# Performance work log

Hardware: AMD Instinct MI355X
Metric: run time of the kernel (lower is better)

Reference implementation:

```python
import jax, jax.numpy as jnp
import numpy as np
import math

C = 128
A_SCALES = [2.0, 4.0, 8.0]
A_RATIOS = [0.5, 1.0, 2.0]
STRIDES = [4, 8, 16, 32, 64]
NA = len(A_SCALES) * len(A_RATIOS)
IMG = 1024
N = 2
NMS_THRESH = 0.7
NUM_PRE = 6000
NUM_POST = 300
SCALE_CLIP = math.log(1000.0 / 16.0)


def base_anchors(stride):
    c = stride / 2.0
    a = []
    for s in A_SCALES:
        for r in A_RATIOS:
            h = stride * s * math.sqrt(r)
            w = stride * s * math.sqrt(1.0 / r)
            a.append((c - h / 2.0, c - w / 2.0, c + h / 2.0, c + w / 2.0))
    return np.array(a, dtype=np.float32)  # [NA,4] yxyx


def shifted_anchors(stride, H, W):
    base = jnp.asarray(base_anchors(stride))
    gy = jnp.arange(H, dtype=jnp.float32) * stride
    gx = jnp.arange(W, dtype=jnp.float32) * stride
    grid = jnp.stack(jnp.meshgrid(gy, gx, indexing='ij'), axis=-1)  # [H,W,2]
    shift = jnp.concatenate([grid, grid], axis=-1)  # [H,W,4]
    return (base[None, None] + shift[:, :, None]).reshape(-1, 4)  # [H*W*NA,4]


def conv(x, w, b, pad):
    y = jax.lax.conv_general_dilated(x, w, (1, 1), pad, dimension_numbers=('NCHW', 'OIHW', 'NCHW'))
    return y + b[None, :, None, None]


def head(x, w1, b1, wobj, bobj, wbbx, bbbx):
    h = jax.nn.relu(conv(x, w1, b1, 'SAME'))
    obj = conv(h, wobj, bobj, 'VALID')  # [N,NA,H,W]
    bbx = conv(h, wbbx, bbbx, 'VALID')  # [N,4*NA,H,W]
    n = x.shape[0]
    obj = obj.transpose(0, 2, 3, 1).reshape(n, -1)       # (h,w,anchor) order
    bbx = bbx.transpose(0, 2, 3, 1).reshape(n, -1, 4)
    return obj, bbx


def shift_boxes(anchors, deltas):
    yx = (anchors[..., :2] + anchors[..., 2:]) * 0.5
    hw = anchors[..., 2:] - anchors[..., :2]
    yx_o = yx + deltas[..., :2] * hw
    hw_o = hw * jnp.exp(jnp.minimum(deltas[..., 2:], SCALE_CLIP))
    return jnp.concatenate([yx_o - 0.5 * hw_o, yx_o + 0.5 * hw_o], axis=-1)


def nms_single(boxes, scores):
    # greedy hard NMS; boxes [P,4] yxyx, scores [P]; fixed NUM_POST outputs
    areas = (boxes[:, 2] - boxes[:, 0]) * (boxes[:, 3] - boxes[:, 1])

    def step(active, _):
        masked = jnp.where(active, scores, -jnp.inf)
        i = jnp.argmax(masked)
        ok = active[i]
        tl = jnp.maximum(boxes[i, :2], boxes[:, :2])
        br = jnp.minimum(boxes[i, 2:], boxes[:, 2:])
        inter = jnp.clip(br[:, 0] - tl[:, 0], 0.0) * jnp.clip(br[:, 1] - tl[:, 1], 0.0)
        iou = inter / (areas[i] + areas - inter + 1e-9)
        active = active & (iou <= NMS_THRESH)
        return active, (jnp.where(ok, i, 0), ok)

    _, (idx, valid) = jax.lax.scan(step, jnp.ones(boxes.shape[0], bool), None, length=NUM_POST)
    return idx, valid


def forward(x0, x1, x2, x3, x4, w1, b1, wobj, bobj, wbbx, bbbx, valid_size):
    feats = [x0, x1, x2, x3, x4]
    objs, bbxs, ancs = [], [], []
    for f, s in zip(feats, STRIDES):
        o, b = head(f, w1, b1, wobj, bobj, wbbx, bbbx)
        objs.append(o)
        bbxs.append(b)
        ancs.append(shifted_anchors(s, f.shape[2], f.shape[3]))
    obj = jnp.concatenate(objs, axis=1)        # [N,M]
    bbx = jnp.concatenate(bbxs, axis=1)        # [N,M,4]
    anchors = jnp.concatenate(ancs, axis=0)    # [M,4]
    boxes = shift_boxes(anchors[None], bbx)    # [N,M,4]
    h = valid_size[:, 0].astype(boxes.dtype)[:, None]
    w = valid_size[:, 1].astype(boxes.dtype)[:, None]
    boxes = jnp.stack([jnp.clip(boxes[..., 0], 0.0, h),
                       jnp.clip(boxes[..., 1], 0.0, w),
                       jnp.clip(boxes[..., 2], 0.0, h),
                       jnp.clip(boxes[..., 3], 0.0, w)], axis=-1)
    k = min(boxes.shape[1], NUM_PRE)
    top_scores, top_idx = jax.lax.top_k(obj, k)                     # per-image topk
    top_boxes = jnp.take_along_axis(boxes, top_idx[..., None], axis=1)
    idx, valid = jax.vmap(nms_single)(jax.lax.stop_gradient(top_boxes),
                                      jax.lax.stop_gradient(top_scores))
    props = jnp.take_along_axis(top_boxes, idx[..., None], axis=1)  # [N,NUM_POST,4]
    props = props * valid[..., None].astype(props.dtype)            # zero-pad invalid
    return props, valid


def setup_inputs() -> dict:
    key = jax.random.key(0)
    ks = jax.random.split(key, 8)
    sizes = [IMG // s for s in STRIDES]
    inp = {}
    for i, hw in enumerate(sizes):
        inp['x%d' % i] = jax.random.normal(ks[i], (N, C, hw, hw), jnp.float32)
    inp['w1'] = jax.random.normal(ks[5], (C, C, 3, 3), jnp.float32) * 0.05
    inp['b1'] = jnp.zeros((C,), jnp.float32)
    inp['wobj'] = jax.random.normal(ks[6], (NA, C, 1, 1), jnp.float32) * 0.05
    inp['bobj'] = jnp.zeros((NA,), jnp.float32)
    inp['wbbx'] = jax.random.normal(ks[7], (4 * NA, C, 1, 1), jnp.float32) * 0.05
    inp['bbbx'] = jnp.zeros((4 * NA,), jnp.float32)
    inp['valid_size'] = jnp.array([[IMG, IMG]] * N, jnp.int32)
    return inp


def reference(x0, x1, x2, x3, x4, w1, b1, wobj, bobj, wbbx, bbbx, valid_size):
    return forward(x0, x1, x2, x3, x4, w1, b1, wobj, bobj, wbbx, bbbx, valid_size)
```

## Files before the change

kernel.cpp:

```cpp
#include <hip/hip_runtime.h>
#include <stdint.h>
#include <math.h>

#define M_TOT 785664
#define NPRE  6000
#define NPOST 300
#define CAP   8192
#define NWORDS 94
#define ROWW   96
#define NPAD   6016

__device__ __forceinline__ uint32_t okey(float f) {
    uint32_t u = __float_as_uint(f);
    return (u & 0x80000000u) ? ~u : (u | 0x80000000u);
}

__device__ __forceinline__ void gload_lds16(const float* g, float* l) {
    __builtin_amdgcn_global_load_lds(
        (__attribute__((address_space(1))) void*)g,
        (__attribute__((address_space(3))) void*)l,
        16, 0, 0);
}

__global__ void k_zero(uint32_t* p, int n) {
    int i = blockIdx.x * blockDim.x + threadIdx.x;
    if (i < n) p[i] = 0u;
}

__global__ void k_wt(const float* __restrict__ w1, float* __restrict__ wt) {
    int i = blockIdx.x * 256 + threadIdx.x;
    if (i >= 128 * 128 * 9) return;
    int co = i / 1152; int r = i % 1152; int ci = r / 9; int tap = r % 9;
    wt[ci * 1152 + tap * 128 + co] = w1[i];
}

__global__ __launch_bounds__(512) void k_conv(
    const float* __restrict__ x0, const float* __restrict__ x1,
    const float* __restrict__ x2, const float* __restrict__ x3,
    const float* __restrict__ x4,
    const float* __restrict__ wt, const float* __restrict__ b1,
    const float* __restrict__ wobj, const float* __restrict__ bobj,
    const float* __restrict__ wbbx, const float* __restrict__ bbbx,
    float* __restrict__ sc, float* __restrict__ dl)
{
    __shared__ __attribute__((aligned(16))) float sx[8][18][20];
    __shared__ __attribute__((aligned(16))) float sw[8 * 9 * 128];

    int b = blockIdx.x, L = 0;
    if (b >= 512) { b -= 512; L = 1;
        if (b >= 128) { b -= 128; L = 2;
            if (b >= 32) { b -= 32; L = 3;
                if (b >= 8) { b -= 8; L = 4; } } } }
    const float* xs = (L == 0) ? x0 : (L == 1) ? x1 : (L == 2) ? x2 : (L == 3) ? x3 : x4;
    const int scoff_[5] = {0, 589824, 737280, 774144, 783360};
    int Wl = 256 >> L; int Hl = Wl; int HW = Wl * Wl;
    int tpiSh = 8 - 2 * L;
    int n  = b >> tpiSh;
    int r  = b & ((1 << tpiSh) - 1);
    int txSh = 4 - L;
    int ty0 = r >> txSh, tx0 = r & ((1 << txSh) - 1);
    int y0 = ty0 << 4, x0c = tx0 << 4;
    const float* xin = xs + (size_t)n * 128 * HW;

    int t = threadIdx.x;
    int tx = t & 15;
    int ty = t >> 4;
    int py = ty >> 1, px = (ty & 1) << 3;

    uint32_t soff[6];
    float xvv[6];
#pragma unroll
    for (int k = 0; k < 6; ++k) {
        int i = t + (k << 9);
        uint32_t off = 0xFFFFFFFFu;
        if (i < 2880) {
            int ci = i / 360; int rm = i % 360; int rr = rm / 20; int cc = rm % 20;
            int gy = y0 - 1 + rr, gx = x0c - 1 + cc;
            if (cc < 18 && gy >= 0 && gy < Hl && gx >= 0 && gx < Wl)
                off = (uint32_t)(ci * HW + gy * Wl + gx);
        }
        soff[k] = off;
    }
    float* sxf = (float*)sx;
    float* swf = (float*)sw;

    float acc0[4][8], acc1[4][8];
#pragma unroll
    for (int c = 0; c < 4; ++c)
#pragma unroll
        for (int e = 0; e < 8; ++e) { acc0[c][e] = 0.f; acc1[c][e] = 0.f; }

#pragma unroll
    for (int k = 0; k < 6; ++k)
        xvv[k] = (soff[k] != 0xFFFFFFFFu) ? xin[soff[k]] : 0.f;
    {
        const float* wsrc = wt;
#pragma unroll
        for (int k = 0; k < 5; ++k) {
            int i = t + (k << 9);
            if (i < 2304) gload_lds16(wsrc + 4 * i, swf + 4 * i);
        }
    }
#pragma unroll
    for (int k = 0; k < 6; ++k) { int i = t + (k << 9); if (i < 2880) sxf[i] = xvv[k]; }
    __syncthreads();

    for (int s = 0; s < 16; ++s) {
        if (s < 15) {
            size_t xb = (size_t)(s + 1) * 8 * HW;
#pragma unroll
            for (int k = 0; k < 6; ++k)
                xvv[k] = (soff[k] != 0xFFFFFFFFu) ? xin[xb + soff[k]] : 0.f;
        }

#pragma unroll 1
        for (int ci = 0; ci < 8; ++ci) {
#pragma unroll
            for (int dy = 0; dy < 3; ++dy) {
                const float* xr = &sx[ci][py + dy][px];
                float4 xa = *(const float4*)(xr);
                float4 xb = *(const float4*)(xr + 4);
                float4 xc = *(const float4*)(xr + 8);
                float win[12] = {xa.x, xa.y, xa.z, xa.w, xb.x, xb.y, xb.z, xb.w,
                                 xc.x, xc.y, xc.z, xc.w};
#pragma unroll
                for (int dx = 0; dx < 3; ++dx) {
                    const float* wr = &sw[(ci * 9 + dy * 3 + dx) * 128 + tx * 4];
                    float4 wa = *(const float4*)(wr);
                    float4 wb = *(const float4*)(wr + 64);
                    float wva[4] = {wa.x, wa.y, wa.z, wa.w};
                    float wvb[4] = {wb.x, wb.y, wb.z, wb.w};
#pragma unroll
                    for (int e = 0; e < 8; ++e) {
                        float xv = win[e + dx];
#pragma unroll
                        for (int c = 0; c < 4; ++c) {
                            acc0[c][e] = fmaf(wva[c], xv, acc0[c][e]);
                            acc1[c][e] = fmaf(wvb[c], xv, acc1[c][e]);
                        }
                    }
                }
            }
        }

        if (s < 15) {
            __syncthreads();
            {
                const float* wsrc = wt + (size_t)(s + 1) * 8 * 1152;
#pragma unroll
                for (int k = 0; k < 5; ++k) {
                    int i = t + (k << 9);
                    if (i < 2304) gload_lds16(wsrc + 4 * i, swf + 4 * i);
                }
            }
#pragma unroll
            for (int k = 0; k < 6; ++k) { int i = t + (k << 9); if (i < 2880) sxf[i] = xvv[k]; }
            __syncthreads();
        }
    }

#pragma unroll
    for (int c = 0; c < 4; ++c) {
        float ba = b1[tx * 4 + c];
        float bb = b1[64 + tx * 4 + c];
#pragma unroll
        for (int e = 0; e < 8; ++e) {
            float v0 = acc0[c][e] + ba;
            float v1 = acc1[c][e] + bb;
            acc0[c][e] = v0 > 0.f ? v0 : 0.f;
            acc1[c][e] = v1 > 0.f ? v1 : 0.f;
        }
    }

    int gy = y0 + py;
    size_t ppos = (size_t)gy * Wl + x0c + px;
    size_t scbase = (size_t)n * M_TOT + scoff_[L];
    size_t dlbase = (size_t)n * 4 * (size_t)M_TOT + 4 * (size_t)scoff_[L];
    for (int a = 0; a < 45; ++a) {
        const float* wp = (a < 9) ? (wobj + (size_t)a * 128) : (wbbx + (size_t)(a - 9) * 128);
        float4 wa = *(const float4*)(wp + tx * 4);
        float4 wb = *(const float4*)(wp + 64 + tx * 4);
        float wva[4] = {wa.x, wa.y, wa.z, wa.w};
        float wvb[4] = {wb.x, wb.y, wb.z, wb.w};
        float p[8];
#pragma unroll
        for (int e = 0; e < 8; ++e) p[e] = 0.f;
#pragma unroll
        for (int c = 0; c < 4; ++c)
#pragma unroll
            for (int e = 0; e < 8; ++e) {
                p[e] = fmaf(wva[c], acc0[c][e], p[e]);
                p[e] = fmaf(wvb[c], acc1[c][e], p[e]);
            }
#pragma unroll
        for (int mm = 1; mm < 16; mm <<= 1)
#pragma unroll
            for (int e = 0; e < 8; ++e)
                p[e] += __shfl_xor(p[e], mm, 64);
        if (tx == 0) {
            float bias = (a < 9) ? bobj[a] : bbbx[a - 9];
            float4 o0 = make_float4(p[0] + bias, p[1] + bias, p[2] + bias, p[3] + bias);
            float4 o1 = make_float4(p[4] + bias, p[5] + bias, p[6] + bias, p[7] + bias);
            float* dst = (a < 9) ? (sc + scbase + (size_t)a * HW + ppos)
                                 : (dl + dlbase + (size_t)(a - 9) * HW + ppos);
            *(float4*)dst = o0;
            *(float4*)(dst + 4) = o1;
        }
    }
}

__global__ __launch_bounds__(256) void k_hist(const float* __restrict__ sc,
                                              uint32_t* __restrict__ hist) {
    __shared__ uint32_t lh[8192];
    int n = blockIdx.y;
    for (int i = threadIdx.x; i < 8192; i += 256) lh[i] = 0u;
    __syncthreads();
    const float* s = sc + (size_t)n * M_TOT;
    int stride = gridDim.x * 256;
    for (int i = blockIdx.x * 256 + threadIdx.x; i < M_TOT; i += stride)
        atomicAdd(&lh[okey(s[i]) >> 19], 1u);
    __syncthreads();
    for (int i = threadIdx.x; i < 8192; i += 256) {
        uint32_t v = lh[i];
        if (v) atomicAdd(&hist[n * 8192 + i], v);
    }
}

__global__ void k_subhist(const float* __restrict__ sc, const uint32_t* __restrict__ ctrl,
                          uint32_t* __restrict__ subh) {
    int i = blockIdx.x * blockDim.x + threadIdx.x;
    int stride = gridDim.x * blockDim.x;
    for (; i < 2 * M_TOT; i += stride) {
        int n = i >= M_TOT;
        uint32_t k = okey(sc[i]);
        if ((k >> 19) == ctrl[n * 8 + 0])
            atomicAdd(&subh[n * 8192 + ((k >> 6) & 0x1FFFu)], 1u);
    }
}

__global__ void k_scan(const uint32_t* __restrict__ hist, uint32_t* __restrict__ ctrl, int phase) {
    int n = blockIdx.x;
    const uint32_t* h = hist + n * 8192;
    uint32_t* c = ctrl + n * 8;
    __shared__ uint32_t tp[256];
    int t = threadIdx.x;
    uint32_t s = 0;
    for (int r = 0; r < 32; ++r) s += h[8191 - (t * 32 + r)];
    tp[t] = s;
    __syncthreads();
    if (t == 0) {
        uint32_t run = (phase == 0) ? 0u : c[1];
        for (int i = 0; i < 256; ++i) { uint32_t v = tp[i]; tp[i] = run; run += v; }
    }
    __syncthreads();
    uint32_t cum = tp[t];
    for (int r = 0; r < 32; ++r) {
        int j = 8191 - (t * 32 + r);
        uint32_t cc = h[j];
        if (cum < 6000u && cum + cc >= 6000u) {
            if (phase == 0) { c[0] = (uint32_t)j; c[1] = cum; }
            else            { c[2] = (c[0] << 19) | ((uint32_t)j << 6); }
        }
        cum += cc;
    }
}

__global__ void k_compact(const float* __restrict__ sc, uint32_t* __restrict__ ctrl,
                          uint64_t* __restrict__ cand) {
    int i = blockIdx.x * blockDim.x + threadIdx.x;
    int stride = gridDim.x * blockDim.x;
    const int scoff_[5] = {0, 589824, 737280, 774144, 783360};
    int lane = threadIdx.x & 63;
    for (; i < 2 * M_TOT; i += stride) {
        int n = i >= M_TOT;
        int q = n ? (i - M_TOT) : i;
        uint32_t k = okey(sc[i]);
        bool hit = (k >= ctrl[n * 8 + 2]);
        unsigned long long m = __ballot(hit);
        if (m) {
            int leader = __builtin_ctzll(m);
            uint32_t base = 0;
            if (lane == leader) base = atomicAdd(&ctrl[n * 8 + 3], (uint32_t)__popcll(m));
            base = (uint32_t)__shfl((int)base, leader, 64);
            if (hit) {
                uint32_t slot = base + (uint32_t)__popcll(m & ((1ull << lane) - 1ull));
                if (slot < CAP) {
                    int Lq = (q < 589824) ? 0 : (q < 737280) ? 1 : (q < 774144) ? 2
                            : (q < 783360) ? 3 : 4;
                    int r = q - scoff_[Lq];
                    int sh = 16 - 2 * Lq;
                    int a = r >> sh;
                    int pos = r & ((1 << sh) - 1);
                    uint32_t mm = (uint32_t)(scoff_[Lq] + pos * 9 + a);
                    cand[(size_t)n * CAP + slot] = ((uint64_t)k << 32) | (uint32_t)(~mm);
                }
            }
        }
    }
}

__global__ __launch_bounds__(256) void k_rank(const uint64_t* __restrict__ cand,
                                              const uint32_t* __restrict__ ctrl,
                                              uint64_t* __restrict__ sorted) {
    __shared__ uint64_t chunk[2048];
    int n = blockIdx.y;
    uint32_t cnt = ctrl[n * 8 + 3];
    if (cnt > CAP) cnt = CAP;
    const uint64_t* cb = cand + (size_t)n * CAP;
    uint64_t* sb = sorted + (size_t)n * CAP;
    int i = blockIdx.x * 256 + threadIdx.x;
    uint64_t key = (i < (int)cnt) ? cb[i] : 0ull;
    uint32_t rank = 0;
    for (uint32_t base = 0; base < cnt; base += 2048) {
        __syncthreads();
        for (int j = threadIdx.x; j < 2048; j += 256) {
            uint32_t idx = base + (uint32_t)j;
            chunk[j] = (idx < cnt) ? cb[idx] : 0ull;
        }
        __syncthreads();
        uint32_t lim = cnt - base; if (lim > 2048u) lim = 2048u;
        for (uint32_t j = 0; j < lim; ++j) rank += (chunk[j] > key) ? 1u : 0u;
    }
    if (i < (int)cnt && rank < CAP) sb[rank] = key;
}

__global__ void k_decode(const uint64_t* __restrict__ cand, const float* __restrict__ dl,
                         const int* __restrict__ vsz, float* __restrict__ boxes,
                         unsigned long long* __restrict__ degm) {
    int i = blockIdx.x * 256 + threadIdx.x;
    if (i >= 2 * NPRE) return;
    int n = i / NPRE, rk = i % NPRE;
    const int scoff_[5] = {0, 589824, 737280, 774144, 783360};
    uint64_t pk = cand[(size_t)n * CAP + rk];
    uint32_t m = ~(uint32_t)(pk & 0xFFFFFFFFull);
    int Lq = (m < 589824u) ? 0 : (m < 737280u) ? 1 : (m < 774144u) ? 2 : (m < 783360u) ? 3 : 4;
    int r = (int)m - scoff_[Lq];
    int pos = r / 9;
    int a = r - pos * 9;
    int Wl = 256 >> Lq;
    int y = pos >> (8 - Lq);
    int xx = pos & (Wl - 1);
    float stridef = (float)(4 << Lq);
    double sD = (double)(2 << (a / 3));
    double rD = ((a % 3) == 0) ? 0.5 : ((a % 3) == 1) ? 1.0 : 2.0;
    double hD = ((double)stridef * sD) * sqrt(rD);
    double wD = ((double)stridef * sD) * sqrt(1.0 / rD);
    double cD = (double)stridef / 2.0;
    float y1b = (float)(cD - hD / 2.0);
    float x1b = (float)(cD - wD / 2.0);
    float y2b = (float)(cD + hD / 2.0);
    float x2b = (float)(cD + wD / 2.0);
    float gy = (float)y * stridef;
    float gx = (float)xx * stridef;
    float ay1 = __fadd_rn(y1b, gy), ax1 = __fadd_rn(x1b, gx);
    float ay2 = __fadd_rn(y2b, gy), ax2 = __fadd_rn(x2b, gx);
    float cy = __fmul_rn(__fadd_rn(ay1, ay2), 0.5f);
    float cx = __fmul_rn(__fadd_rn(ax1, ax2), 0.5f);
    float ah = __fsub_rn(ay2, ay1);
    float aw = __fsub_rn(ax2, ax1);
    size_t HWl = (size_t)Wl * Wl;
    size_t db = (size_t)n * 4 * M_TOT + 4 * (size_t)scoff_[Lq] + (size_t)pos;
    float dy_ = dl[db + (size_t)(a * 4 + 0) * HWl];
    float dx_ = dl[db + (size_t)(a * 4 + 1) * HWl];
    float dh_ = dl[db + (size_t)(a * 4 + 2) * HWl];
    float dw_ = dl[db + (size_t)(a * 4 + 3) * HWl];
    float yo = __fadd_rn(cy, __fmul_rn(dy_, ah));
    float xo = __fadd_rn(cx, __fmul_rn(dx_, aw));
    const float SCLIPf = 4.135166556742356f;
    float ho = __fmul_rn(ah, (float)exp((double)fminf(dh_, SCLIPf)));
    float wo = __fmul_rn(aw, (float)exp((double)fminf(dw_, SCLIPf)));
    float hf = (float)vsz[n * 2 + 0], wf = (float)vsz[n * 2 + 1];
    float y1 = fminf(fmaxf(__fsub_rn(yo, __fmul_rn(0.5f, ho)), 0.f), hf);
    float x1 = fminf(fmaxf(__fsub_rn(xo, __fmul_rn(0.5f, wo)), 0.f), wf);
    float y2 = fminf(fmaxf(__fadd_rn(yo, __fmul_rn(0.5f, ho)), 0.f), hf);
    float x2 = fminf(fmaxf(__fadd_rn(xo, __fmul_rn(0.5f, wo)), 0.f), wf);
    *(float4*)(boxes + ((size_t)n * NPAD + rk) * 4) = make_float4(y1, x1, y2, x2);
    float area = __fmul_rn(__fsub_rn(y2, y1), __fsub_rn(x2, x1));
    float selfiou = __fdiv_rn(area, __fadd_rn(area, 1e-9f));
    if (!(selfiou > 0.7f))
        atomicOr(&degm[(size_t)n * ROWW + (rk >> 6)], 1ull << (rk & 63));
}

__global__ __launch_bounds__(256) void k_iou(const float* __restrict__ boxes,
                                             uint64_t* __restrict__ ioum) {
    int n = blockIdx.y;
    int i = blockIdx.x * 4 + (threadIdx.x >> 6);
    int lane = threadIdx.x & 63;
    const float* bsrc = boxes + (size_t)n * NPAD * 4;
    float4 bi = *(const float4*)(bsrc + (size_t)i * 4);
    float ai = __fmul_rn(__fsub_rn(bi.z, bi.x), __fsub_rn(bi.w, bi.y));
    uint64_t* row = ioum + ((size_t)n * NPAD + i) * ROWW;
    int w0 = i >> 6;
    for (int w = lane; w < w0; w += 64) row[w] = 0ull;
    for (int w = w0; w < NWORDS; ++w) {
        int j = (w << 6) | lane;
        bool pred = false;
        if (j > i && j < NPRE) {
            float4 bj = *(const float4*)(bsrc + (size_t)j * 4);
            float aj = __fmul_rn(__fsub_rn(bj.z, bj.x), __fsub_rn(bj.w, bj.y));
            float ty = fmaxf(bi.x, bj.x), tx2 = fmaxf(bi.y, bj.y);
            float by = fminf(bi.z, bj.z), bx2 = fminf(bi.w, bj.w);
            float ih = fmaxf(__fsub_rn(by, ty), 0.f), iw = fmaxf(__fsub_rn(bx2, tx2), 0.f);
            float inter = __fmul_rn(ih, iw);
            float den = __fadd_rn(__fsub_rn(__fadd_rn(ai, aj), inter), 1e-9f);
            float iou = __fdiv_rn(inter, den);
            pred = iou > 0.7f;
        }
        unsigned long long msk = __ballot(pred);
        if (lane == 0) row[w] = (uint64_t)msk;
    }
}

__global__ __launch_bounds__(64) void k_nms(const float* __restrict__ boxes,
                                            const uint64_t* __restrict__ ioum,
                                            const unsigned long long* __restrict__ degm,
                                            float* __restrict__ out) {
    int n = blockIdx.x;
    __shared__ uint64_t sup[NWORDS];
    __shared__ uint64_t deg[NWORDS];
    __shared__ int keepl[NPOST];
    int lane = threadIdx.x;
    for (int w = lane; w < NWORDS; w += 64) {
        sup[w] = 0ull;
        deg[w] = degm[(size_t)n * ROWW + w];
    }
    __syncthreads();
    int kept = 0;
    bool stop = false;
    for (int w = 0; w < NWORDS && kept < NPOST && !stop; ++w) {
        uint64_t vmask = (w == NWORDS - 1) ? ((1ull << 48) - 1ull) : ~0ull;
        uint64_t avail = (~sup[w]) & vmask;
        while (avail && kept < NPOST) {
            int bpos = __builtin_ctzll(avail);
            int i = (w << 6) | bpos;
            const uint64_t* row = ioum + ((size_t)n * NPAD + i) * ROWW;
            uint64_t r0 = row[lane];
            uint64_t r1 = (lane < NWORDS - 64) ? row[64 + lane] : 0ull;
            if (lane == 0) keepl[kept] = i;
            kept++;
            if ((deg[w] >> bpos) & 1ull) {
                if (lane == 0) { for (int k2 = kept; k2 < NPOST; ++k2) keepl[k2] = i; }
                kept = NPOST;
                stop = true;
                break;
            }
            sup[lane] |= r0;
            if (lane < NWORDS - 64) sup[64 + lane] |= r1;
            __syncthreads();
            avail = (~sup[w]) & vmask & ~((2ull << bpos) - 1ull);
        }
    }
    __syncthreads();
    for (int k = lane; k < NPOST; k += 64) {
        float4 bx = make_float4(0.f, 0.f, 0.f, 0.f);
        float vf = 0.f;
        if (k < kept) {
            int i = keepl[k];
            bx = *(const float4*)(boxes + ((size_t)n * NPAD + i) * 4);
            vf = 1.f;
        }
        *(float4*)(out + (size_t)n * 1200 + (size_t)k * 4) = bx;
        out[2400 + n * 300 + k] = vf;
    }
}

__global__ __launch_bounds__(256) void k_diag(const uint32_t* __restrict__ ctrl,
                                              const uint64_t* __restrict__ sorted,
                                              const float* __restrict__ boxes,
                                              float* __restrict__ out) {
    __shared__ unsigned sfl;
    if (threadIdx.x == 0) sfl = 0u;
    __syncthreads();
    unsigned fl = 0;
    for (int n = 0; n < 2; ++n) {
        if (threadIdx.x == 0) {
            uint32_t cnt = ctrl[n * 8 + 3];
            if (cnt < 6000u || cnt > (uint32_t)CAP) fl |= 1u << n;
        }
        for (int r = threadIdx.x + 1; r < NPRE; r += 256)
            if (sorted[(size_t)n * CAP + r - 1] <= sorted[(size_t)n * CAP + r])
                fl |= 4u << n;
        for (int r = threadIdx.x; r < NPRE * 4; r += 256) {
            float v = boxes[(size_t)n * NPAD * 4 + r];
            if (!(v >= 0.0f && v <= 1024.0f)) fl |= 16u << n;
        }
    }
    if (fl) atomicOr(&sfl, fl);
    __syncthreads();
    if (threadIdx.x == 0 && sfl) out[0] = 65536.0f * (float)(1u + sfl);
}

extern "C" void kernel_launch(void* const* d_in, const int* in_sizes, int n_in,
                              void* d_out, int out_size, void* d_ws, size_t ws_size,
                              hipStream_t stream) {
    (void)out_size; (void)ws_size;
    static const int want[12] = {16777216, 4194304, 1048576, 262144, 65536,
                                 147456, 128, 1152, 9, 4608, 36, 4};
    const void* p[12];
    for (int k = 0; k < 12; ++k) p[k] = d_in[k];
    bool pos_ok = (n_in >= 12);
    for (int k = 0; k < 12 && pos_ok; ++k) if (in_sizes[k] != want[k]) pos_ok = false;
    if (!pos_ok) {
        for (int k = 0; k < 12; ++k)
            for (int j = 0; j < n_in; ++j)
                if (in_sizes[j] == want[k]) { p[k] = d_in[j]; break; }
    }
    const float* x0   = (const float*)p[0];
    const float* x1   = (const float*)p[1];
    const float* x2   = (const float*)p[2];
    const float* x3   = (const float*)p[3];
    const float* x4   = (const float*)p[4];
    const float* w1   = (const float*)p[5];
    const float* b1   = (const float*)p[6];
    const float* wobj = (const float*)p[7];
    const float* bobj = (const float*)p[8];
    const float* wbbx = (const float*)p[9];
    const float* bbbx = (const float*)p[10];
    const int*   vsz  = (const int*)p[11];
    float* out = (float*)d_out;

    size_t off = 0;
    char* base = (char*)d_ws;
    auto carve = [&](size_t bytes) -> void* {
        void* q = base + off;
        off += (bytes + 255) & ~(size_t)255;
        return q;
    };
    float*    SC     = (float*)carve((size_t)2 * M_TOT * 4);
    float*    DL     = (float*)carve((size_t)2 * M_TOT * 16);
    float*    WT     = (float*)carve((size_t)147456 * 4);
    uint32_t* HIST   = (uint32_t*)carve((size_t)16384 * 4);
    uint32_t* SUBH   = (uint32_t*)carve((size_t)16384 * 4);
    uint32_t* CTRL   = (uint32_t*)carve((size_t)64 * 4);
    unsigned long long* DEGM = (unsigned long long*)carve((size_t)2 * ROWW * 8);
    uint64_t* CAND   = (uint64_t*)carve((size_t)2 * CAP * 8);
    uint64_t* SORTED = (uint64_t*)carve((size_t)2 * CAP * 8);
    float*    BOXES  = (float*)carve((size_t)2 * NPAD * 16);
    uint64_t* IOUM   = (uint64_t*)carve((size_t)2 * NPAD * ROWW * 8);

    int zn = (int)(((char*)CAND - (char*)HIST) / 4);
    k_zero<<<(zn + 255) / 256, 256, 0, stream>>>(HIST, zn);
    k_wt<<<(147456 + 255) / 256, 256, 0, stream>>>(w1, WT);
    k_conv<<<682, 512, 0, stream>>>(x0, x1, x2, x3, x4, WT, b1,
                                    wobj, bobj, wbbx, bbbx, SC, DL);
    k_hist<<<dim3(256, 2), 256, 0, stream>>>(SC, HIST);
    k_scan<<<2, 256, 0, stream>>>(HIST, CTRL, 0);
    k_subhist<<<1024, 256, 0, stream>>>(SC, CTRL, SUBH);
    k_scan<<<2, 256, 0, stream>>>(SUBH, CTRL, 1);
    k_compact<<<1024, 256, 0, stream>>>(SC, CTRL, CAND);
    k_rank<<<dim3(CAP / 256, 2), 256, 0, stream>>>(CAND, CTRL, SORTED);
    k_decode<<<(2 * NPRE + 255) / 256, 256, 0, stream>>>(SORTED, DL, vsz, BOXES, DEGM);
    k_iou<<<dim3(NPRE / 4, 2), 256, 0, stream>>>(BOXES, IOUM);
    k_nms<<<2, 64, 0, stream>>>(BOXES, IOUM, DEGM, out);
    k_diag<<<1, 256, 0, stream>>>(CTRL, SORTED, BOXES, out);
}
```

Before: 1.072 ms.

## Remap conv threads to one pixel each and read weights from global memory

```diff
diff --git a/kernel.cpp b/kernel.cpp
--- a/kernel.cpp
+++ b/kernel.cpp
@@ -15,13 +15,6 @@
     return (u & 0x80000000u) ? ~u : (u | 0x80000000u);
 }
 
-__device__ __forceinline__ void gload_lds16(const float* g, float* l) {
-    __builtin_amdgcn_global_load_lds(
-        (__attribute__((address_space(1))) void*)g,
-        (__attribute__((address_space(3))) void*)l,
-        16, 0, 0);
-}
-
 __global__ void k_zero(uint32_t* p, int n) {
     int i = blockIdx.x * blockDim.x + threadIdx.x;
     if (i < n) p[i] = 0u;
@@ -33,6 +26,23 @@
     int co = i / 1152; int r = i % 1152; int ci = r / 9; int tap = r % 9;
     wt[ci * 1152 + tap * 128 + co] = w1[i];
 }
+
+#define FMAJ(XV, WR)                                                        \
+    {                                                                       \
+        _Pragma("unroll")                                                   \
+        for (int j = 0; j < 8; ++j) {                                       \
+            float4 wl = *(const float4*)((WR) + 4 * j);                     \
+            float4 wh = *(const float4*)((WR) + 64 + 4 * j);                \
+            accl[j][0] = fmaf(wl.x, (XV), accl[j][0]);                      \
+            accl[j][1] = fmaf(wl.y, (XV), accl[j][1]);                      \
+            accl[j][2] = fmaf(wl.z, (XV), accl[j][2]);                      \
+            accl[j][3] = fmaf(wl.w, (XV), accl[j][3]);                      \
+            acch[j][0] = fmaf(wh.x, (XV), acch[j][0]);                      \
+            acch[j][1] = fmaf(wh.y, (XV), acch[j][1]);                      \
+            acch[j][2] = fmaf(wh.z, (XV), acch[j][2]);                      \
+            acch[j][3] = fmaf(wh.w, (XV), acch[j][3]);                      \
+        }                                                                   \
+    }
 
 __global__ __launch_bounds__(512) void k_conv(
     const float* __restrict__ x0, const float* __restrict__ x1,
@@ -44,7 +54,7 @@
     float* __restrict__ sc, float* __restrict__ dl)
 {
     __shared__ __attribute__((aligned(16))) float sx[8][18][20];
-    __shared__ __attribute__((aligned(16))) float sw[8 * 9 * 128];
+    __shared__ __attribute__((aligned(16))) float hb[9][256];
 
     int b = blockIdx.x, L = 0;
     if (b >= 512) { b -= 512; L = 1;
@@ -63,9 +73,10 @@
     const float* xin = xs + (size_t)n * 128 * HW;
 
     int t = threadIdx.x;
-    int tx = t & 15;
-    int ty = t >> 4;
-    int py = ty >> 1, px = (ty & 1) << 3;
+    int p = t & 255;
+    int g = t >> 8;
+    int gu = __builtin_amdgcn_readfirstlane(g);
+    int py = p >> 4, px = p & 15;
 
     uint32_t soff[6];
     float xvv[6];
@@ -82,25 +93,16 @@
         soff[k] = off;
     }
     float* sxf = (float*)sx;
-    float* swf = (float*)sw;
-
-    float acc0[4][8], acc1[4][8];
-#pragma unroll
-    for (int c = 0; c < 4; ++c)
-#pragma unroll
-        for (int e = 0; e < 8; ++e) { acc0[c][e] = 0.f; acc1[c][e] = 0.f; }
+
+    float accl[8][4], acch[8][4];
+#pragma unroll
+    for (int j = 0; j < 8; ++j)
+#pragma unroll
+        for (int c = 0; c < 4; ++c) { accl[j][c] = 0.f; acch[j][c] = 0.f; }
 
 #pragma unroll
     for (int k = 0; k < 6; ++k)
         xvv[k] = (soff[k] != 0xFFFFFFFFu) ? xin[soff[k]] : 0.f;
-    {
-        const float* wsrc = wt;
-#pragma unroll
-        for (int k = 0; k < 5; ++k) {
-            int i = t + (k << 9);
-            if (i < 2304) gload_lds16(wsrc + 4 * i, swf + 4 * i);
-        }
-    }
 #pragma unroll
     for (int k = 0; k < 6; ++k) { int i = t + (k << 9); if (i < 2880) sxf[i] = xvv[k]; }
     __syncthreads();
@@ -113,46 +115,23 @@
                 xvv[k] = (soff[k] != 0xFFFFFFFFu) ? xin[xb + soff[k]] : 0.f;
         }
 
+        const float* wts = wt + (size_t)s * 9216 + (gu << 5);
 #pragma unroll 1
         for (int ci = 0; ci < 8; ++ci) {
 #pragma unroll
             for (int dy = 0; dy < 3; ++dy) {
-                const float* xr = &sx[ci][py + dy][px];
-                float4 xa = *(const float4*)(xr);
-                float4 xb = *(const float4*)(xr + 4);
-                float4 xc = *(const float4*)(xr + 8);
-                float win[12] = {xa.x, xa.y, xa.z, xa.w, xb.x, xb.y, xb.z, xb.w,
-                                 xc.x, xc.y, xc.z, xc.w};
-#pragma unroll
-                for (int dx = 0; dx < 3; ++dx) {
-                    const float* wr = &sw[(ci * 9 + dy * 3 + dx) * 128 + tx * 4];
-                    float4 wa = *(const float4*)(wr);
-                    float4 wb = *(const float4*)(wr + 64);
-                    float wva[4] = {wa.x, wa.y, wa.z, wa.w};
-                    float wvb[4] = {wb.x, wb.y, wb.z, wb.w};
-#pragma unroll
-                    for (int e = 0; e < 8; ++e) {
-                        float xv = win[e + dx];
-#pragma unroll
-                        for (int c = 0; c < 4; ++c) {
-                            acc0[c][e] = fmaf(wva[c], xv, acc0[c][e]);
-                            acc1[c][e] = fmaf(wvb[c], xv, acc1[c][e]);
-                        }
-                    }
-                }
+                float xq0 = sx[ci][py + dy][px];
+                float xq1 = sx[ci][py + dy][px + 1];
+                float xq2 = sx[ci][py + dy][px + 2];
+                const float* wrow = wts + (ci * 9 + dy * 3) * 128;
+                FMAJ(xq0, wrow);
+                FMAJ(xq1, wrow + 128);
+                FMAJ(xq2, wrow + 256);
             }
         }
 
         if (s < 15) {
             __syncthreads();
-            {
-                const float* wsrc = wt + (size_t)(s + 1) * 8 * 1152;
-#pragma unroll
-                for (int k = 0; k < 5; ++k) {
-                    int i = t + (k << 9);
-                    if (i < 2304) gload_lds16(wsrc + 4 * i, swf + 4 * i);
-                }
-            }
 #pragma unroll
             for (int k = 0; k < 6; ++k) { int i = t + (k << 9); if (i < 2880) sxf[i] = xvv[k]; }
             __syncthreads();
@@ -160,52 +139,63 @@
     }
 
 #pragma unroll
-    for (int c = 0; c < 4; ++c) {
-        float ba = b1[tx * 4 + c];
-        float bb = b1[64 + tx * 4 + c];
-#pragma unroll
-        for (int e = 0; e < 8; ++e) {
-            float v0 = acc0[c][e] + ba;
-            float v1 = acc1[c][e] + bb;
-            acc0[c][e] = v0 > 0.f ? v0 : 0.f;
-            acc1[c][e] = v1 > 0.f ? v1 : 0.f;
-        }
-    }
-
-    int gy = y0 + py;
-    size_t ppos = (size_t)gy * Wl + x0c + px;
+    for (int j = 0; j < 8; ++j)
+#pragma unroll
+        for (int c = 0; c < 4; ++c) {
+            float bl = b1[(gu << 5) + 4 * j + c];
+            float bh = b1[64 + (gu << 5) + 4 * j + c];
+            float v0 = accl[j][c] + bl;
+            float v1 = acch[j][c] + bh;
+            accl[j][c] = v0 > 0.f ? v0 : 0.f;
+            acch[j][c] = v1 > 0.f ? v1 : 0.f;
+        }
+
+    size_t ppos = (size_t)(y0 + py) * Wl + x0c + px;
     size_t scbase = (size_t)n * M_TOT + scoff_[L];
     size_t dlbase = (size_t)n * 4 * (size_t)M_TOT + 4 * (size_t)scoff_[L];
-    for (int a = 0; a < 45; ++a) {
-        const float* wp = (a < 9) ? (wobj + (size_t)a * 128) : (wbbx + (size_t)(a - 9) * 128);
-        float4 wa = *(const float4*)(wp + tx * 4);
-        float4 wb = *(const float4*)(wp + 64 + tx * 4);
-        float wva[4] = {wa.x, wa.y, wa.z, wa.w};
-        float wvb[4] = {wb.x, wb.y, wb.z, wb.w};
-        float p[8];
-#pragma unroll
-        for (int e = 0; e < 8; ++e) p[e] = 0.f;
-#pragma unroll
-        for (int c = 0; c < 4; ++c)
-#pragma unroll
-            for (int e = 0; e < 8; ++e) {
-                p[e] = fmaf(wva[c], acc0[c][e], p[e]);
-                p[e] = fmaf(wvb[c], acc1[c][e], p[e]);
+#pragma unroll 1
+    for (int a0 = 0; a0 < 45; a0 += 9) {
+        float A[9];
+#pragma unroll
+        for (int aa = 0; aa < 9; ++aa) {
+            int a = a0 + aa;
+            const float* wp = (a < 9) ? (wobj + (size_t)a * 128)
+                                      : (wbbx + (size_t)(a - 9) * 128);
+            const float* wq0 = wp + (gu << 5);
+            float pj[8];
+#pragma unroll
+            for (int j = 0; j < 8; ++j) {
+                const float* wq = wq0 + 4 * j;
+                float4 wl = *(const float4*)(wq);
+                float4 wh = *(const float4*)(wq + 64);
+                float pp = 0.f;
+                pp = fmaf(wl.x, accl[j][0], pp); pp = fmaf(wh.x, acch[j][0], pp);
+                pp = fmaf(wl.y, accl[j][1], pp); pp = fmaf(wh.y, acch[j][1], pp);
+                pp = fmaf(wl.z, accl[j][2], pp); pp = fmaf(wh.z, acch[j][2], pp);
+                pp = fmaf(wl.w, accl[j][3], pp); pp = fmaf(wh.w, acch[j][3], pp);
+                pj[j] = pp;
             }
-#pragma unroll
-        for (int mm = 1; mm < 16; mm <<= 1)
-#pragma unroll
-            for (int e = 0; e < 8; ++e)
-                p[e] += __shfl_xor(p[e], mm, 64);
-        if (tx == 0) {
-            float bias = (a < 9) ? bobj[a] : bbbx[a - 9];
-            float4 o0 = make_float4(p[0] + bias, p[1] + bias, p[2] + bias, p[3] + bias);
-            float4 o1 = make_float4(p[4] + bias, p[5] + bias, p[6] + bias, p[7] + bias);
-            float* dst = (a < 9) ? (sc + scbase + (size_t)a * HW + ppos)
-                                 : (dl + dlbase + (size_t)(a - 9) * HW + ppos);
-            *(float4*)dst = o0;
-            *(float4*)(dst + 4) = o1;
-        }
+            A[aa] = ((pj[0] + pj[1]) + (pj[2] + pj[3]))
+                  + ((pj[4] + pj[5]) + (pj[6] + pj[7]));
+        }
+        if (g == 1) {
+#pragma unroll
+            for (int aa = 0; aa < 9; ++aa) hb[aa][p] = A[aa];
+        }
+        __syncthreads();
+        if (g == 0) {
+#pragma unroll
+            for (int aa = 0; aa < 9; ++aa) {
+                int a = a0 + aa;
+                float S = A[aa] + hb[aa][p];
+                float bias = (a < 9) ? bobj[a] : bbbx[a - 9];
+                float o = S + bias;
+                float* dst = (a < 9) ? (sc + scbase + (size_t)a * HW + ppos)
+                                     : (dl + dlbase + (size_t)(a - 9) * HW + ppos);
+                *dst = o;
+            }
+        }
+        __syncthreads();
     }
 }
 
```

Result: slower. 4.201 ms, median of 2 (+291.8%).
